# Optimization experiments

Hardware: AMD Instinct MI355X
Metric: run time of the kernel (lower is better)

Reference implementation:

```python
import jax, jax.numpy as jnp
import numpy as np

N_CAMP = 50
DAYS = 365          # execution_duration
N_STATES = 3
BASIS = 1e-10


def setup_inputs() -> dict:
    key = jax.random.key(0)
    k1, k2, k3, k4, k5 = jax.random.split(key, 5)
    adstock = jax.random.uniform(k1, (4096, N_CAMP, DAYS + 1), dtype=jnp.float32)
    mu = jax.random.normal(k2, (3,), dtype=jnp.float32)
    beta = jax.random.normal(k3, (3 * N_CAMP,), dtype=jnp.float32)
    init_prob = jax.random.normal(k4, (1,), dtype=jnp.float32)
    click_prob = jax.random.normal(k5, (1,), dtype=jnp.float32)
    return {"adstock": adstock, "mu": mu, "beta": beta,
            "init_prob": init_prob, "click_prob": click_prob}


def make_transition_matrix(mu, beta, adstock, basis=BASIS):
    b = adstock.shape[0]
    # [N_camp, 4]: zero column + reshaped betas
    beta_r = jnp.concatenate(
        [jnp.zeros((N_CAMP, 1), adstock.dtype), beta.reshape(N_CAMP, 3)], axis=1)
    # tensordot over campaign axis: [b, days, 4]
    O_beta = jnp.einsum('bcd,ck->bdk', adstock[:, :, 1:], beta_r)
    # [-inf, mu0, mu1, mu2]; exp(-inf)=0 kills the (0,0) slot exactly as in TF
    mu_full = jnp.concatenate([jnp.full((1,), -jnp.inf, dtype=mu.dtype), mu])
    mp = (mu_full[None, None, :] + O_beta).reshape(b, DAYS, N_STATES - 1, -1)
    num = jnp.exp(mp)                      # [b, D, 2, 2]
    den = 1.0 + jnp.sum(num, axis=3)       # [b, D, 2]
    main_diag = jnp.concatenate(
        [1.0 / den, jnp.ones((b, DAYS, 1), den.dtype)], axis=-1)   # [b, D, 3]
    lower_diag = jnp.concatenate(
        [num[:, :, 1:, 0] / den[:, :, 1:],
         jnp.zeros((b, DAYS, 1), den.dtype)], axis=-1)             # [b, D, 2]
    upper_diag = num[:, :, :, 1] / den                              # [b, D, 2]
    Q = jnp.zeros((b, DAYS, N_STATES, N_STATES), den.dtype)
    i = jnp.arange(N_STATES)
    Q = Q.at[..., i, i].set(main_diag)                 # main diagonal
    Q = Q.at[..., i[1:], i[:-1]].set(lower_diag)       # k = -1
    Q = Q.at[..., i[:-1], i[1:]].set(upper_diag)       # k = +1
    return jnp.maximum(Q, basis)


def reference(adstock, mu, beta, init_prob, click_prob):
    Q = make_transition_matrix(mu, beta, adstock)
    return Q, jax.nn.sigmoid(init_prob), jax.nn.sigmoid(click_prob)
```

## Files before the change

kernel.cpp:

```cpp
#include <hip/hip_runtime.h>

#define N_CAMP 50
#define DAYS   365
#define ROW    366
#define BASIS  1e-10f
#define BATCH  4096
#define NTHR   384
#define CPG    10
#define NGROUP (N_CAMP / CPG)
#define GROUP_F4 (CPG * ROW / 4)

__global__ __launch_bounds__(NTHR)
void transition_prob_kernel(const float* __restrict__ adstock,
                            const float* __restrict__ mu,
                            const float* __restrict__ beta,
                            const float* __restrict__ init_prob,
                            const float* __restrict__ click_prob,
                            float* __restrict__ out)
{
    __shared__ float sA[CPG * ROW];
    __shared__ float sb0[N_CAMP];
    __shared__ float sb1[N_CAMP];
    __shared__ float sb2[N_CAMP];
    __shared__ float smu[3];

    const int tid = threadIdx.x;
    const int b   = blockIdx.x;

    if (tid < 3 * N_CAMP) {
        const int c = tid / 3;
        const int k = tid % 3;
        const float v = beta[tid];
        if (k == 0) sb0[c] = v;
        else if (k == 1) sb1[c] = v;
        else sb2[c] = v;
    }
    if (tid < 3) smu[tid] = mu[tid];

    if (b == 0 && tid == NTHR - 1) {
        const size_t base = (size_t)BATCH * DAYS * 9;
        out[base + 0] = 1.0f / (1.0f + __expf(-init_prob[0]));
        out[base + 1] = 1.0f / (1.0f + __expf(-click_prob[0]));
    }

    const float4* rowbase = reinterpret_cast<const float4*>(
        adstock + (size_t)b * (N_CAMP * ROW));

    const int d = tid;
    float o1 = 0.f, o2 = 0.f, o3 = 0.f;

    for (int g = 0; g < NGROUP; ++g) {
        __syncthreads();

        const float4* src = rowbase + g * GROUP_F4;
        float4* dstv = reinterpret_cast<float4*>(sA);
#pragma unroll
        for (int i = tid; i < GROUP_F4; i += NTHR) {
            dstv[i] = src[i];
        }
        __syncthreads();

        if (d < DAYS) {
            const int c0 = g * CPG;
#pragma unroll
            for (int cc = 0; cc < CPG; ++cc) {
                const float a  = sA[cc * ROW + d + 1];
                o1 = fmaf(a, sb0[c0 + cc], o1);
                o2 = fmaf(a, sb1[c0 + cc], o2);
                o3 = fmaf(a, sb2[c0 + cc], o3);
            }
        }
    }

    if (d < DAYS) {
        const float e1 = __expf(smu[0] + o1);
        const float e2 = __expf(smu[1] + o2);
        const float e3 = __expf(smu[2] + o3);
        const float inv0 = __frcp_rn(1.0f + e1);
        const float inv1 = __frcp_rn(1.0f + e2 + e3);

        float* qo = out + ((size_t)b * DAYS + d) * 9;
        qo[0] = fmaxf(inv0,      BASIS);
        qo[1] = fmaxf(e1 * inv0, BASIS);
        qo[2] = BASIS;
        qo[3] = fmaxf(e2 * inv1, BASIS);
        qo[4] = fmaxf(inv1,      BASIS);
        qo[5] = fmaxf(e3 * inv1, BASIS);
        qo[6] = BASIS;
        qo[7] = BASIS;
        qo[8] = 1.0f;
    }
}

extern "C" void kernel_launch(void* const* d_in, const int* in_sizes, int n_in,
                              void* d_out, int out_size, void* d_ws, size_t ws_size,
                              hipStream_t stream)
{
    const float* adstock    = (const float*)d_in[0];
    const float* mu         = (const float*)d_in[1];
    const float* beta       = (const float*)d_in[2];
    const float* init_prob  = (const float*)d_in[3];
    const float* click_prob = (const float*)d_in[4];
    float* out = (float*)d_out;

    transition_prob_kernel<<<dim3(BATCH), dim3(NTHR), 0, stream>>>(
        adstock, mu, beta, init_prob, click_prob, out);
}
```

Measured before the change: 80.73 us.

## Read adstock directly from global memory and use nontemporal output stores

Drops the shared-memory staging of adstock in groups of ten campaigns, along with the two barriers per group. Each thread now reads its own day column straight from global memory across all 50 campaigns, with the loop unrolled by 10. All output writes become nontemporal stores to avoid polluting the cache. Loads stay coalesced across threads but lose the aligned float4 vector loads, because rows start at an offset of one element.

Result: faster. 67.96 us (-15.8%).

```diff
diff --git a/kernel.cpp b/kernel.cpp
--- a/kernel.cpp
+++ b/kernel.cpp
@@ -6,9 +6,6 @@
 #define BASIS  1e-10f
 #define BATCH  4096
 #define NTHR   384
-#define CPG    10
-#define NGROUP (N_CAMP / CPG)
-#define GROUP_F4 (CPG * ROW / 4)
 
 __global__ __launch_bounds__(NTHR)
 void transition_prob_kernel(const float* __restrict__ adstock,
@@ -18,7 +15,6 @@
                             const float* __restrict__ click_prob,
                             float* __restrict__ out)
 {
-    __shared__ float sA[CPG * ROW];
     __shared__ float sb0[N_CAMP];
     __shared__ float sb1[N_CAMP];
     __shared__ float sb2[N_CAMP];
@@ -36,43 +32,27 @@
         else sb2[c] = v;
     }
     if (tid < 3) smu[tid] = mu[tid];
+    __syncthreads();
 
     if (b == 0 && tid == NTHR - 1) {
         const size_t base = (size_t)BATCH * DAYS * 9;
-        out[base + 0] = 1.0f / (1.0f + __expf(-init_prob[0]));
-        out[base + 1] = 1.0f / (1.0f + __expf(-click_prob[0]));
+        __builtin_nontemporal_store(1.0f / (1.0f + __expf(-init_prob[0])), &out[base + 0]);
+        __builtin_nontemporal_store(1.0f / (1.0f + __expf(-click_prob[0])), &out[base + 1]);
     }
 
-    const float4* rowbase = reinterpret_cast<const float4*>(
-        adstock + (size_t)b * (N_CAMP * ROW));
+    const int d = tid;
+    if (d < DAYS) {
+        const float* arow = adstock + (size_t)b * (N_CAMP * ROW) + (d + 1);
 
-    const int d = tid;
-    float o1 = 0.f, o2 = 0.f, o3 = 0.f;
+        float o1 = 0.f, o2 = 0.f, o3 = 0.f;
+#pragma unroll 10
+        for (int c = 0; c < N_CAMP; ++c) {
+            const float a = arow[(size_t)c * ROW];
+            o1 = fmaf(a, sb0[c], o1);
+            o2 = fmaf(a, sb1[c], o2);
+            o3 = fmaf(a, sb2[c], o3);
+        }
 
-    for (int g = 0; g < NGROUP; ++g) {
-        __syncthreads();
-
-        const float4* src = rowbase + g * GROUP_F4;
-        float4* dstv = reinterpret_cast<float4*>(sA);
-#pragma unroll
-        for (int i = tid; i < GROUP_F4; i += NTHR) {
-            dstv[i] = src[i];
-        }
-        __syncthreads();
-
-        if (d < DAYS) {
-            const int c0 = g * CPG;
-#pragma unroll
-            for (int cc = 0; cc < CPG; ++cc) {
-                const float a  = sA[cc * ROW + d + 1];
-                o1 = fmaf(a, sb0[c0 + cc], o1);
-                o2 = fmaf(a, sb1[c0 + cc], o2);
-                o3 = fmaf(a, sb2[c0 + cc], o3);
-            }
-        }
-    }
-
-    if (d < DAYS) {
         const float e1 = __expf(smu[0] + o1);
         const float e2 = __expf(smu[1] + o2);
         const float e3 = __expf(smu[2] + o3);
@@ -80,15 +60,15 @@
         const float inv1 = __frcp_rn(1.0f + e2 + e3);
 
         float* qo = out + ((size_t)b * DAYS + d) * 9;
-        qo[0] = fmaxf(inv0,      BASIS);
-        qo[1] = fmaxf(e1 * inv0, BASIS);
-        qo[2] = BASIS;
-        qo[3] = fmaxf(e2 * inv1, BASIS);
-        qo[4] = fmaxf(inv1,      BASIS);
-        qo[5] = fmaxf(e3 * inv1, BASIS);
-        qo[6] = BASIS;
-        qo[7] = BASIS;
-        qo[8] = 1.0f;
+        __builtin_nontemporal_store(fmaxf(inv0,      BASIS), &qo[0]);
+        __builtin_nontemporal_store(fmaxf(e1 * inv0, BASIS), &qo[1]);
+        __builtin_nontemporal_store(BASIS,                   &qo[2]);
+        __builtin_nontemporal_store(fmaxf(e2 * inv1, BASIS), &qo[3]);
+        __builtin_nontemporal_store(fmaxf(inv1,      BASIS), &qo[4]);
+        __builtin_nontemporal_store(fmaxf(e3 * inv1, BASIS), &qo[5]);
+        __builtin_nontemporal_store(BASIS,                   &qo[6]);
+        __builtin_nontemporal_store(BASIS,                   &qo[7]);
+        __builtin_nontemporal_store(1.0f,                    &qo[8]);
     }
 }
 
```
